# Optimization experiments

Hardware: AMD Instinct MI355X
Metric: run time of the kernel (lower is better)

Reference implementation:

```python
import jax, jax.numpy as jnp
import numpy as np

NUM_CLASSES = 19
RMI_RADIUS = 3
POOL_SIZE = 3
POOL_STRIDE = 3
IGNORE_INDEX = 255
LOSS_WEIGHT = 1.0


def _avg_pool_nchw(x, k, s):
    # torch F.avg_pool2d with padding=k//2, count_include_pad=True
    p = k // 2
    summed = jax.lax.reduce_window(
        x, 0.0, jax.lax.add,
        window_dimensions=(1, 1, k, k),
        window_strides=(1, 1, s, s),
        padding=[(0, 0), (0, 0), (p, p), (p, p)])
    return summed / float(k * k)


def _map_get_pairs(labels, probs, radius):
    h, w = labels.shape[2], labels.shape[3]
    nh, nw = h - radius + 1, w - radius + 1
    la = jnp.stack([labels[:, :, y:y + nh, x:x + nw]
                    for y in range(radius) for x in range(radius)], axis=2)
    pr = jnp.stack([probs[:, :, y:y + nh, x:x + nw]
                    for y in range(radius) for x in range(radius)], axis=2)
    return la, pr  # (N, C, r*r, nh, nw)


def _log_det_by_cholesky(mat):
    chol = jnp.linalg.cholesky(mat)
    diag = jnp.diagonal(chol, axis1=-2, axis2=-1)
    return 2.0 * jnp.sum(jnp.log(diag + 1e-8), axis=-1)


def _rmi_lower_bound(labels_4d, probs_4d):
    labels_4d = _avg_pool_nchw(labels_4d, POOL_SIZE, POOL_STRIDE)
    probs_4d = _avg_pool_nchw(probs_4d, POOL_SIZE, POOL_STRIDE)
    la, pr = _map_get_pairs(labels_4d, probs_4d, RMI_RADIUS)
    N, C, D = la.shape[:3]
    la = la.reshape(N, C, D, -1)   # (N, C, D, M)
    pr = pr.reshape(N, C, D, -1)
    M = la.shape[-1]
    la = la - la.mean(axis=-1, keepdims=True)
    pr = pr - pr.mean(axis=-1, keepdims=True)
    la_cov = jnp.einsum('ncdm,ncem->ncde', la, la) / M
    pr_cov = jnp.einsum('ncdm,ncem->ncde', pr, pr) / M
    pr_la_cov = jnp.einsum('ncdm,ncem->ncde', pr, la) / M
    eye = jnp.eye(D, dtype=la_cov.dtype)
    la_cov_inv = jnp.linalg.inv(la_cov + eye * 1e-5)
    appro_var = pr_cov - jnp.einsum('ncde,ncef,ncgf->ncdg',
                                    pr_la_cov, la_cov_inv, pr_la_cov)
    appro_var = appro_var + eye * 1e-6
    rmi_per_class = 0.5 * _log_det_by_cholesky(appro_var)  # (N, C)
    rmi_per_class = rmi_per_class.mean(axis=0)             # (C,)
    return jnp.sum(rmi_per_class) / NUM_CLASSES


def setup_inputs() -> dict:
    key = jax.random.key(0)
    k1, k2 = jax.random.split(key)
    cls_score = jax.random.normal(k1, (4, 19, 512, 512), dtype=jnp.float32)
    label = jax.random.randint(k2, (4, 512, 512), 0, NUM_CLASSES, dtype=jnp.int64)
    return {"cls_score": cls_score, "label": label}


def reference(cls_score, label):
    probs = jax.nn.softmax(cls_score.astype(jnp.float32), axis=1)
    valid = (label >= 0) & (label < NUM_CLASSES) & (label != IGNORE_INDEX)
    lbl = jnp.where(valid, label, 0)
    onehot = jax.nn.one_hot(lbl, NUM_CLASSES, dtype=jnp.float32)
    onehot = jnp.transpose(onehot, (0, 3, 1, 2))  # (N, C, H, W)
    vmask = valid[:, None, :, :].astype(jnp.float32)
    onehot = onehot * vmask
    probs = probs * vmask
    loss = _rmi_lower_bound(onehot, probs)
    return LOSS_WEIGHT * loss
```

## Files before the change

### kernel.cpp

```cpp
#include <hip/hip_runtime.h>
#include <math.h>

#define NBATCH 4
#define NCLS   19
#define HWDIM  512
#define HW     (512 * 512)
#define PH     171
#define PP2    (171 * 171)
#define NHW    169
#define MM     (169 * 169)
#define ZSPLIT 2

__global__ __launch_bounds__(512) void stage1_pool(
    const float* __restrict__ cls, const int* __restrict__ label,
    float* __restrict__ P, float* __restrict__ L) {
  int n  = blockIdx.x / PH;
  int ph = blockIdx.x - n * PH;
  int col = threadIdx.x;

  float accP[NCLS], accL[NCLS];
#pragma unroll
  for (int c = 0; c < NCLS; ++c) { accP[c] = 0.f; accL[c] = 0.f; }

#pragma unroll
  for (int i = 0; i < 3; ++i) {
    int r = 3 * ph - 1 + i;
    if (r < 0 || r >= HWDIM) continue;
    int lb = label[((size_t)n * HWDIM + r) * HWDIM + col];
    const float* base = cls + (size_t)n * NCLS * HW + (size_t)r * HWDIM + col;
    float v[NCLS];
    float mx = -INFINITY;
#pragma unroll
    for (int c = 0; c < NCLS; ++c) {
      v[c] = base[(size_t)c * HW];
      mx = fmaxf(mx, v[c]);
    }
    float se = 0.f;
#pragma unroll
    for (int c = 0; c < NCLS; ++c) {
      v[c] = expf(v[c] - mx);
      se += v[c];
    }
    if (lb >= 0 && lb < NCLS) {
      float inv = 1.f / se;
#pragma unroll
      for (int c = 0; c < NCLS; ++c) {
        accP[c] += v[c] * inv;
        accL[c] += (lb == c) ? 1.f : 0.f;
      }
    }
  }

  __shared__ float xbP[4][516];
  __shared__ float xbL[4][516];
  const float inv9 = 1.f / 9.f;
#pragma unroll
  for (int c0 = 0; c0 < NCLS; c0 += 4) {
    int nc_round = (NCLS - c0) < 4 ? (NCLS - c0) : 4;
#pragma unroll
    for (int cc = 0; cc < 4; ++cc) {
      if (cc < nc_round) {
        xbP[cc][1 + col] = accP[(c0 + cc) < NCLS ? (c0 + cc) : 0];
        xbL[cc][1 + col] = accL[(c0 + cc) < NCLS ? (c0 + cc) : 0];
        if (col == 0) { xbP[cc][0] = 0.f; xbL[cc][0] = 0.f; }
      }
    }
    __syncthreads();
    if (col < PH) {
      int pw = col;
#pragma unroll
      for (int cc = 0; cc < 4; ++cc) {
        if (cc < nc_round) {
          int c = c0 + cc;
          float sP = xbP[cc][3 * pw] + xbP[cc][3 * pw + 1] + xbP[cc][3 * pw + 2];
          float sL = xbL[cc][3 * pw] + xbL[cc][3 * pw + 1] + xbL[cc][3 * pw + 2];
          size_t o = ((size_t)(n * NCLS + c)) * PP2 + (size_t)ph * PH + pw;
          P[o] = sP * inv9;
          L[o] = sL * inv9;
        }
      }
    }
    __syncthreads();
  }
}

template <int PART>
__device__ __forceinline__ void mom_body(
    int nc, int z, const float* __restrict__ P, const float* __restrict__ L,
    float* __restrict__ covp, float* red) {
  constexpr int NA  = (PART == 0) ? 63 : (PART == 1 ? 45 : 81);
  constexpr int OFF = (PART == 0) ? 0  : (PART == 1 ? 63 : 108);
  const float* Pp = P + (size_t)nc * PP2;
  const float* Lp = L + (size_t)nc * PP2;

  float acc[NA];
#pragma unroll
  for (int k = 0; k < NA; ++k) acc[k] = 0.f;

  int task = threadIdx.x;
  if (task < 3 * NHW) {
    int ysub = task / NHW;
    int xx   = task - ysub * NHW;
    int base = z * 85;
    int rt   = (z == 0) ? 85 : (NHW - 85);
    int y0 = base + (rt * ysub) / 3;
    int y1 = base + (rt * (ysub + 1)) / 3;

    float wp[9], wl[9];
#pragma unroll
    for (int dy = 0; dy < 2; ++dy) {
#pragma unroll
      for (int dx = 0; dx < 3; ++dx) {
        wp[dy * 3 + dx] = Pp[(y0 + dy) * PH + xx + dx];
        if (PART != 1) wl[dy * 3 + dx] = Lp[(y0 + dy) * PH + xx + dx];
      }
    }
    for (int y = y0; y < y1; ++y) {
#pragma unroll
      for (int dx = 0; dx < 3; ++dx) {
        wp[6 + dx] = Pp[(y + 2) * PH + xx + dx];
        if (PART != 1) wl[6 + dx] = Lp[(y + 2) * PH + xx + dx];
      }
      if (PART == 0) {
#pragma unroll
        for (int d = 0; d < 9; ++d) {
          acc[d]     += wl[d];
          acc[9 + d] += wp[d];
        }
        int k = 18;
#pragma unroll
        for (int d = 0; d < 9; ++d)
#pragma unroll
          for (int e = d; e < 9; ++e) { acc[k] += wl[d] * wl[e]; ++k; }
      } else if (PART == 1) {
        int k = 0;
#pragma unroll
        for (int d = 0; d < 9; ++d)
#pragma unroll
          for (int e = d; e < 9; ++e) { acc[k] += wp[d] * wp[e]; ++k; }
      } else {
#pragma unroll
        for (int d = 0; d < 9; ++d)
#pragma unroll
          for (int e = 0; e < 9; ++e) acc[d * 9 + e] += wp[d] * wl[e];
      }
#pragma unroll
      for (int t = 0; t < 6; ++t) {
        wp[t] = wp[t + 3];
        if (PART != 1) wl[t] = wl[t + 3];
      }
    }
  }

  int lane = threadIdx.x & 63;
  int wid  = threadIdx.x >> 6;
#pragma unroll
  for (int k = 0; k < NA; ++k) {
    float v = acc[k];
#pragma unroll
    for (int o = 32; o > 0; o >>= 1) v += __shfl_down(v, o, 64);
    if (lane == 0) red[wid * NA + k] = v;
  }
  __syncthreads();
  if (threadIdx.x < NA) {
    float s = 0.f;
#pragma unroll
    for (int w = 0; w < 8; ++w) s += red[w * NA + threadIdx.x];
    covp[((size_t)z * NBATCH * NCLS + nc) * 192 + OFF + threadIdx.x] = s;
  }
}

__global__ __launch_bounds__(512) void stage2_mom(
    const float* __restrict__ P, const float* __restrict__ L,
    float* __restrict__ covp) {
  __shared__ float red[8 * 81];
  int nc = blockIdx.x;
  int z  = blockIdx.z;
  if (blockIdx.y == 0)      mom_body<0>(nc, z, P, L, covp, red);
  else if (blockIdx.y == 1) mom_body<1>(nc, z, P, L, covp, red);
  else                      mom_body<2>(nc, z, P, L, covp, red);
}

__global__ __launch_bounds__(64) void stage3_rmi(float* __restrict__ covp) {
  int nc  = blockIdx.x;
  int tid = threadIdx.x;
  const float* s0 = covp + (size_t)nc * 192;
  const float* s1 = covp + ((size_t)NBATCH * NCLS + nc) * 192;
  __shared__ double lc[81], pc[81], plc[81], mla[9], mpr[9];
  const double Minv = 1.0 / (double)MM;
#define LDM(k) ((double)s0[k] + (double)s1[k])

  if (tid < 9)       mla[tid]     = LDM(tid) * Minv;
  else if (tid < 18) mpr[tid - 9] = LDM(tid) * Minv;
  __syncthreads();

  for (int e = tid; e < 81; e += 64) {
    int r = e / 9, c = e - 9 * (e / 9);
    int lo = r < c ? r : c, hi = r < c ? c : r;
    int k = lo * 9 - lo * (lo - 1) / 2 + (hi - lo);
    double a = LDM(18 + k) * Minv - mla[r] * mla[c];
    if (r == c) a += 1e-5;
    lc[e] = a;
    pc[e] = LDM(63 + k) * Minv - mpr[r] * mpr[c];
    plc[e] = LDM(108 + e) * Minv - mpr[r] * mla[c];
  }
  __syncthreads();

  for (int j = 0; j < 9; ++j) {
    if (tid == 0) lc[j * 9 + j] = sqrt(lc[j * 9 + j]);
    __syncthreads();
    if (tid > j && tid < 9) lc[tid * 9 + j] /= lc[j * 9 + j];
    __syncthreads();
    if (tid > j && tid < 9) {
      double lij = lc[tid * 9 + j];
      for (int k = j + 1; k <= tid; ++k) lc[tid * 9 + k] -= lij * lc[k * 9 + j];
    }
    __syncthreads();
  }

  if (tid < 9) {
    int d = tid;
    for (int j = 0; j < 9; ++j) {
      double t = plc[d * 9 + j];
      for (int k = 0; k < j; ++k) t -= plc[d * 9 + k] * lc[j * 9 + k];
      plc[d * 9 + j] = t / lc[j * 9 + j];
    }
  }
  __syncthreads();

  for (int e = tid; e < 81; e += 64) {
    int r = e / 9, c = e - 9 * (e / 9);
    double a = pc[e];
    for (int f = 0; f < 9; ++f) a -= plc[r * 9 + f] * plc[c * 9 + f];
    if (r == c) a += 1e-6;
    pc[e] = a;
  }
  __syncthreads();

  for (int j = 0; j < 9; ++j) {
    if (tid == 0) pc[j * 9 + j] = sqrt(pc[j * 9 + j]);
    __syncthreads();
    if (tid > j && tid < 9) pc[tid * 9 + j] /= pc[j * 9 + j];
    __syncthreads();
    if (tid > j && tid < 9) {
      double lij = pc[tid * 9 + j];
      for (int k = j + 1; k <= tid; ++k) pc[tid * 9 + k] -= lij * pc[k * 9 + j];
    }
    __syncthreads();
  }

  if (tid == 0) {
    double sl = 0.0;
    for (int j = 0; j < 9; ++j) sl += log(pc[j * 9 + j] + 1e-8);
    *(double*)(covp + (size_t)nc * 192 + 190) = sl;
  }
#undef LDM
}

__global__ __launch_bounds__(64) void stage4_reduce(
    const float* __restrict__ covp, float* __restrict__ out) {
  int tid = threadIdx.x;
  double v = 0.0;
  if (tid < NBATCH * NCLS)
    v = *(const double*)(covp + (size_t)tid * 192 + 190);
  if (tid + 64 < NBATCH * NCLS)
    v += *(const double*)(covp + (size_t)(tid + 64) * 192 + 190);
#pragma unroll
  for (int o = 32; o > 0; o >>= 1) v += __shfl_down(v, o, 64);
  if (tid == 0) out[0] = (float)(v / (double)(NBATCH * NCLS));
}

extern "C" void kernel_launch(void* const* d_in, const int* in_sizes, int n_in,
                              void* d_out, int out_size, void* d_ws, size_t ws_size,
                              hipStream_t stream) {
  const float* cls  = (const float*)d_in[0];
  const int* label  = (const int*)d_in[1];
  float* out = (float*)d_out;

  float* P    = (float*)d_ws;
  float* L    = P + (size_t)NBATCH * NCLS * PP2;
  float* covp = L + (size_t)NBATCH * NCLS * PP2;

  stage1_pool<<<NBATCH * PH, 512, 0, stream>>>(cls, label, P, L);
  dim3 g2(NBATCH * NCLS, 3, ZSPLIT);
  stage2_mom<<<g2, 512, 0, stream>>>(P, L, covp);
  stage3_rmi<<<NBATCH * NCLS, 64, 0, stream>>>(covp);
  stage4_reduce<<<1, 64, 0, stream>>>(covp, out);
}
```

Before: 80.44 us.

## Vectorize stage1 softmax loads with float4 and prefetch next row in moment kernel

Stage1 now uses 384 threads, one per (row, 4-column) group, so each thread does float4 loads of the 19 class planes and the label row. The 3x3 pooling is done through shared memory covering all three input rows, one class per iteration. Stage2 prefetches the next window row into registers one iteration ahead to hide global load latency. In exchange, stage1 has more barriers (19 syncs) and each thread holds more registers (19 float4 values).

```diff
diff --git a/kernel.cpp b/kernel.cpp
--- a/kernel.cpp
+++ b/kernel.cpp
@@ -11,74 +11,91 @@
 #define MM     (169 * 169)
 #define ZSPLIT 2
 
-__global__ __launch_bounds__(512) void stage1_pool(
+typedef float f4 __attribute__((ext_vector_type(4)));
+
+__global__ __launch_bounds__(384) void stage1_pool(
     const float* __restrict__ cls, const int* __restrict__ label,
     float* __restrict__ P, float* __restrict__ L) {
-  int n  = blockIdx.x / PH;
-  int ph = blockIdx.x - n * PH;
-  int col = threadIdx.x;
-
-  float accP[NCLS], accL[NCLS];
-#pragma unroll
-  for (int c = 0; c < NCLS; ++c) { accP[c] = 0.f; accL[c] = 0.f; }
-
-#pragma unroll
-  for (int i = 0; i < 3; ++i) {
-    int r = 3 * ph - 1 + i;
-    if (r < 0 || r >= HWDIM) continue;
-    int lb = label[((size_t)n * HWDIM + r) * HWDIM + col];
-    const float* base = cls + (size_t)n * NCLS * HW + (size_t)r * HWDIM + col;
-    float v[NCLS];
-    float mx = -INFINITY;
+  int n   = blockIdx.x / PH;
+  int ph  = blockIdx.x - n * PH;
+  int t   = threadIdx.x;
+  int row = t >> 7;
+  int c4  = (t & 127) << 2;
+
+  int r = 3 * ph - 1 + row;
+  bool rowok = (r >= 0) && (r < HWDIM);
+
+  f4 v[NCLS];
+  f4 mx, se, inv;
+  int lb0 = -1, lb1 = -1, lb2 = -1, lb3 = -1;
+  f4 vmask = {0.f, 0.f, 0.f, 0.f};
+
+  if (rowok) {
+    const int4 lq = *(const int4*)(label + ((size_t)n * HWDIM + r) * HWDIM + c4);
+    lb0 = lq.x; lb1 = lq.y; lb2 = lq.z; lb3 = lq.w;
+    vmask.x = (lb0 >= 0 && lb0 < NCLS) ? 1.f : 0.f;
+    vmask.y = (lb1 >= 0 && lb1 < NCLS) ? 1.f : 0.f;
+    vmask.z = (lb2 >= 0 && lb2 < NCLS) ? 1.f : 0.f;
+    vmask.w = (lb3 >= 0 && lb3 < NCLS) ? 1.f : 0.f;
+
+    const float* base = cls + (size_t)n * NCLS * HW + (size_t)r * HWDIM + c4;
+#pragma unroll
+    for (int c = 0; c < NCLS; ++c)
+      v[c] = *(const f4*)(base + (size_t)c * HW);
+
+    mx = v[0];
+#pragma unroll
+    for (int c = 1; c < NCLS; ++c) {
+#pragma unroll
+      for (int j = 0; j < 4; ++j) mx[j] = fmaxf(mx[j], v[c][j]);
+    }
+    se = (f4){0.f, 0.f, 0.f, 0.f};
 #pragma unroll
     for (int c = 0; c < NCLS; ++c) {
-      v[c] = base[(size_t)c * HW];
-      mx = fmaxf(mx, v[c]);
-    }
-    float se = 0.f;
-#pragma unroll
-    for (int c = 0; c < NCLS; ++c) {
-      v[c] = expf(v[c] - mx);
-      se += v[c];
-    }
-    if (lb >= 0 && lb < NCLS) {
-      float inv = 1.f / se;
-#pragma unroll
-      for (int c = 0; c < NCLS; ++c) {
-        accP[c] += v[c] * inv;
-        accL[c] += (lb == c) ? 1.f : 0.f;
-      }
-    }
-  }
-
-  __shared__ float xbP[4][516];
-  __shared__ float xbL[4][516];
+#pragma unroll
+      for (int j = 0; j < 4; ++j) {
+        v[c][j] = expf(v[c][j] - mx[j]);
+        se[j] += v[c][j];
+      }
+    }
+#pragma unroll
+    for (int j = 0; j < 4; ++j) inv[j] = vmask[j] / se[j];
+  } else {
+#pragma unroll
+    for (int c = 0; c < NCLS; ++c) v[c] = (f4){0.f, 0.f, 0.f, 0.f};
+    inv = (f4){0.f, 0.f, 0.f, 0.f};
+  }
+
+  __shared__ float xbP[3][512];
+  __shared__ float xbL[3][512];
   const float inv9 = 1.f / 9.f;
-#pragma unroll
-  for (int c0 = 0; c0 < NCLS; c0 += 4) {
-    int nc_round = (NCLS - c0) < 4 ? (NCLS - c0) : 4;
-#pragma unroll
-    for (int cc = 0; cc < 4; ++cc) {
-      if (cc < nc_round) {
-        xbP[cc][1 + col] = accP[(c0 + cc) < NCLS ? (c0 + cc) : 0];
-        xbL[cc][1 + col] = accL[(c0 + cc) < NCLS ? (c0 + cc) : 0];
-        if (col == 0) { xbP[cc][0] = 0.f; xbL[cc][0] = 0.f; }
-      }
-    }
-    __syncthreads();
-    if (col < PH) {
-      int pw = col;
-#pragma unroll
-      for (int cc = 0; cc < 4; ++cc) {
-        if (cc < nc_round) {
-          int c = c0 + cc;
-          float sP = xbP[cc][3 * pw] + xbP[cc][3 * pw + 1] + xbP[cc][3 * pw + 2];
-          float sL = xbL[cc][3 * pw] + xbL[cc][3 * pw + 1] + xbL[cc][3 * pw + 2];
-          size_t o = ((size_t)(n * NCLS + c)) * PP2 + (size_t)ph * PH + pw;
-          P[o] = sP * inv9;
-          L[o] = sL * inv9;
-        }
-      }
+  int pw = t;
+
+#pragma unroll
+  for (int c = 0; c < NCLS; ++c) {
+    f4 pv, lv;
+#pragma unroll
+    for (int j = 0; j < 4; ++j) pv[j] = v[c][j] * inv[j];
+    lv.x = (lb0 == c) ? vmask.x : 0.f;
+    lv.y = (lb1 == c) ? vmask.y : 0.f;
+    lv.z = (lb2 == c) ? vmask.z : 0.f;
+    lv.w = (lb3 == c) ? vmask.w : 0.f;
+    *(f4*)&xbP[row][c4] = pv;
+    *(f4*)&xbL[row][c4] = lv;
+    __syncthreads();
+    if (pw < PH) {
+      int x0 = 3 * pw - 1;
+      float sP = 0.f, sL = 0.f;
+#pragma unroll
+      for (int i = 0; i < 3; ++i) {
+        float a = (pw > 0) ? xbP[i][x0] : 0.f;
+        float b = (pw > 0) ? xbL[i][x0] : 0.f;
+        sP += a + xbP[i][x0 + 1] + xbP[i][x0 + 2];
+        sL += b + xbL[i][x0 + 1] + xbL[i][x0 + 2];
+      }
+      size_t o = ((size_t)(n * NCLS + c)) * PP2 + (size_t)ph * PH + pw;
+      P[o] = sP * inv9;
+      L[o] = sL * inv9;
     }
     __syncthreads();
   }
@@ -106,7 +123,7 @@
     int y0 = base + (rt * ysub) / 3;
     int y1 = base + (rt * (ysub + 1)) / 3;
 
-    float wp[9], wl[9];
+    float wp[9], wl[9], pfp[3], pfl[3];
 #pragma unroll
     for (int dy = 0; dy < 2; ++dy) {
 #pragma unroll
@@ -115,11 +132,23 @@
         if (PART != 1) wl[dy * 3 + dx] = Lp[(y0 + dy) * PH + xx + dx];
       }
     }
+#pragma unroll
+    for (int dx = 0; dx < 3; ++dx) {
+      pfp[dx] = Pp[(y0 + 2) * PH + xx + dx];
+      if (PART != 1) pfl[dx] = Lp[(y0 + 2) * PH + xx + dx];
+    }
+
     for (int y = y0; y < y1; ++y) {
 #pragma unroll
       for (int dx = 0; dx < 3; ++dx) {
-        wp[6 + dx] = Pp[(y + 2) * PH + xx + dx];
-        if (PART != 1) wl[6 + dx] = Lp[(y + 2) * PH + xx + dx];
+        wp[6 + dx] = pfp[dx];
+        if (PART != 1) wl[6 + dx] = pfl[dx];
+      }
+      int yn = y + 3; if (yn > PH - 1) yn = PH - 1;
+#pragma unroll
+      for (int dx = 0; dx < 3; ++dx) {
+        pfp[dx] = Pp[yn * PH + xx + dx];
+        if (PART != 1) pfl[dx] = Lp[yn * PH + xx + dx];
       }
       if (PART == 0) {
 #pragma unroll
@@ -145,9 +174,9 @@
           for (int e = 0; e < 9; ++e) acc[d * 9 + e] += wp[d] * wl[e];
       }
 #pragma unroll
-      for (int t = 0; t < 6; ++t) {
-        wp[t] = wp[t + 3];
-        if (PART != 1) wl[t] = wl[t + 3];
+      for (int s = 0; s < 6; ++s) {
+        wp[s] = wp[s + 3];
+        if (PART != 1) wl[s] = wl[s + 3];
       }
     }
   }
@@ -281,7 +310,7 @@
   float* L    = P + (size_t)NBATCH * NCLS * PP2;
   float* covp = L + (size_t)NBATCH * NCLS * PP2;
 
-  stage1_pool<<<NBATCH * PH, 512, 0, stream>>>(cls, label, P, L);
+  stage1_pool<<<NBATCH * PH, 384, 0, stream>>>(cls, label, P, L);
   dim3 g2(NBATCH * NCLS, 3, ZSPLIT);
   stage2_mom<<<g2, 512, 0, stream>>>(P, L, covp);
   stage3_rmi<<<NBATCH * NCLS, 64, 0, stream>>>(covp);
```

Result: slower. 90.57 us (+12.6%).

## Split moment pass into six row bands staged through shared memory

Applied to the files above, without the earlier changes.

The moment-accumulation kernel now divides the 169 output rows into six bands instead of two, which triples the number of blocks. Each block first copies its band of pooled P and L rows (plus a two-row halo) into LDS, and the sliding-window loop then reads from shared memory instead of global memory. The RMI kernel now sums six partial records per (batch, class) instead of two. The aim is to fill more compute units and cut redundant global loads, at the price of about 42KB of LDS per block, a load-then-sync prologue, and more halo rows re-read across bands.

```diff
diff --git a/kernel.cpp b/kernel.cpp
--- a/kernel.cpp
+++ b/kernel.cpp
@@ -9,7 +9,8 @@
 #define PP2    (171 * 171)
 #define NHW    169
 #define MM     (169 * 169)
-#define ZSPLIT 2
+#define ZB     6
+#define HMAX   31
 
 __global__ __launch_bounds__(512) void stage1_pool(
     const float* __restrict__ cls, const int* __restrict__ label,
@@ -86,12 +87,10 @@
 
 template <int PART>
 __device__ __forceinline__ void mom_body(
-    int nc, int z, const float* __restrict__ P, const float* __restrict__ L,
-    float* __restrict__ covp, float* red) {
+    int bw, const float* sP, const float* sL,
+    float* __restrict__ covp, int rec, float* red) {
   constexpr int NA  = (PART == 0) ? 63 : (PART == 1 ? 45 : 81);
   constexpr int OFF = (PART == 0) ? 0  : (PART == 1 ? 63 : 108);
-  const float* Pp = P + (size_t)nc * PP2;
-  const float* Lp = L + (size_t)nc * PP2;
 
   float acc[NA];
 #pragma unroll
@@ -101,25 +100,23 @@
   if (task < 3 * NHW) {
     int ysub = task / NHW;
     int xx   = task - ysub * NHW;
-    int base = z * 85;
-    int rt   = (z == 0) ? 85 : (NHW - 85);
-    int y0 = base + (rt * ysub) / 3;
-    int y1 = base + (rt * (ysub + 1)) / 3;
+    int y0 = (bw * ysub) / 3;
+    int y1 = (bw * (ysub + 1)) / 3;
 
     float wp[9], wl[9];
 #pragma unroll
     for (int dy = 0; dy < 2; ++dy) {
 #pragma unroll
       for (int dx = 0; dx < 3; ++dx) {
-        wp[dy * 3 + dx] = Pp[(y0 + dy) * PH + xx + dx];
-        if (PART != 1) wl[dy * 3 + dx] = Lp[(y0 + dy) * PH + xx + dx];
+        wp[dy * 3 + dx] = sP[(y0 + dy) * PH + xx + dx];
+        if (PART != 1) wl[dy * 3 + dx] = sL[(y0 + dy) * PH + xx + dx];
       }
     }
     for (int y = y0; y < y1; ++y) {
 #pragma unroll
       for (int dx = 0; dx < 3; ++dx) {
-        wp[6 + dx] = Pp[(y + 2) * PH + xx + dx];
-        if (PART != 1) wl[6 + dx] = Lp[(y + 2) * PH + xx + dx];
+        wp[6 + dx] = sP[(y + 2) * PH + xx + dx];
+        if (PART != 1) wl[6 + dx] = sL[(y + 2) * PH + xx + dx];
       }
       if (PART == 0) {
 #pragma unroll
@@ -145,9 +142,9 @@
           for (int e = 0; e < 9; ++e) acc[d * 9 + e] += wp[d] * wl[e];
       }
 #pragma unroll
-      for (int t = 0; t < 6; ++t) {
-        wp[t] = wp[t + 3];
-        if (PART != 1) wl[t] = wl[t + 3];
+      for (int s = 0; s < 6; ++s) {
+        wp[s] = wp[s + 3];
+        if (PART != 1) wl[s] = wl[s + 3];
       }
     }
   }
@@ -166,29 +163,50 @@
     float s = 0.f;
 #pragma unroll
     for (int w = 0; w < 8; ++w) s += red[w * NA + threadIdx.x];
-    covp[((size_t)z * NBATCH * NCLS + nc) * 192 + OFF + threadIdx.x] = s;
+    covp[(size_t)rec * 192 + OFF + threadIdx.x] = s;
   }
 }
 
 __global__ __launch_bounds__(512) void stage2_mom(
     const float* __restrict__ P, const float* __restrict__ L,
     float* __restrict__ covp) {
+  __shared__ float sP[HMAX * PH];
+  __shared__ float sL[HMAX * PH];
   __shared__ float red[8 * 81];
   int nc = blockIdx.x;
+  int part = blockIdx.y;
   int z  = blockIdx.z;
-  if (blockIdx.y == 0)      mom_body<0>(nc, z, P, L, covp, red);
-  else if (blockIdx.y == 1) mom_body<1>(nc, z, P, L, covp, red);
-  else                      mom_body<2>(nc, z, P, L, covp, red);
+  int w0 = (NHW * z) / ZB;
+  int w1 = (NHW * (z + 1)) / ZB;
+  int bw = w1 - w0;
+  int tot = (bw + 2) * PH;
+
+  const float* Pp = P + (size_t)nc * PP2 + (size_t)w0 * PH;
+  const float* Lp = L + (size_t)nc * PP2 + (size_t)w0 * PH;
+  for (int i = threadIdx.x; i < tot; i += 512) {
+    sP[i] = Pp[i];
+    if (part != 1) sL[i] = Lp[i];
+  }
+  __syncthreads();
+
+  int rec = z * (NBATCH * NCLS) + nc;
+  if (part == 0)      mom_body<0>(bw, sP, sL, covp, rec, red);
+  else if (part == 1) mom_body<1>(bw, sP, sL, covp, rec, red);
+  else                mom_body<2>(bw, sP, sL, covp, rec, red);
 }
 
 __global__ __launch_bounds__(64) void stage3_rmi(float* __restrict__ covp) {
   int nc  = blockIdx.x;
   int tid = threadIdx.x;
-  const float* s0 = covp + (size_t)nc * 192;
-  const float* s1 = covp + ((size_t)NBATCH * NCLS + nc) * 192;
   __shared__ double lc[81], pc[81], plc[81], mla[9], mpr[9];
   const double Minv = 1.0 / (double)MM;
-#define LDM(k) ((double)s0[k] + (double)s1[k])
+
+#define LDM(k) ( (double)covp[(size_t)(0 * NBATCH * NCLS + nc) * 192 + (k)] \
+               + (double)covp[(size_t)(1 * NBATCH * NCLS + nc) * 192 + (k)] \
+               + (double)covp[(size_t)(2 * NBATCH * NCLS + nc) * 192 + (k)] \
+               + (double)covp[(size_t)(3 * NBATCH * NCLS + nc) * 192 + (k)] \
+               + (double)covp[(size_t)(4 * NBATCH * NCLS + nc) * 192 + (k)] \
+               + (double)covp[(size_t)(5 * NBATCH * NCLS + nc) * 192 + (k)] )
 
   if (tid < 9)       mla[tid]     = LDM(tid) * Minv;
   else if (tid < 18) mpr[tid - 9] = LDM(tid) * Minv;
@@ -282,7 +300,7 @@
   float* covp = L + (size_t)NBATCH * NCLS * PP2;
 
   stage1_pool<<<NBATCH * PH, 512, 0, stream>>>(cls, label, P, L);
-  dim3 g2(NBATCH * NCLS, 3, ZSPLIT);
+  dim3 g2(NBATCH * NCLS, 3, ZB);
   stage2_mom<<<g2, 512, 0, stream>>>(P, L, covp);
   stage3_rmi<<<NBATCH * NCLS, 64, 0, stream>>>(covp);
   stage4_reduce<<<1, 64, 0, stream>>>(covp, out);
```

Result: slower. 121.1 us (+50.6%).

## Tile moment kernel into 4-wide strips with vector loads and padded rows

Applied to the files above, without the earlier changes.

Stage1 now writes pooled maps with rows padded to 176 floats and zero-fills the pad columns. Stage2 gives each thread a 4-column by band-of-rows tile and reads the 3x6 window with float4/float2 loads, so each loaded row feeds four output columns. It also drops the two-way z split, so stage3 reads one partial instead of summing two. This cuts redundant global loads per output and the extra blocks, but leaves only 228 blocks and raises register pressure from the 18-element windows on top of up to 81 accumulators.

```diff
diff --git a/kernel.cpp b/kernel.cpp
--- a/kernel.cpp
+++ b/kernel.cpp
@@ -6,10 +6,15 @@
 #define HWDIM  512
 #define HW     (512 * 512)
 #define PH     171
-#define PP2    (171 * 171)
+#define PHP    176
+#define PP2A   (171 * 176)
 #define NHW    169
 #define MM     (169 * 169)
-#define ZSPLIT 2
+#define NBAND  11
+#define NSTRIP 43
+
+typedef float f4 __attribute__((ext_vector_type(4)));
+typedef float f2 __attribute__((ext_vector_type(2)));
 
 __global__ __launch_bounds__(512) void stage1_pool(
     const float* __restrict__ cls, const int* __restrict__ label,
@@ -74,11 +79,21 @@
           int c = c0 + cc;
           float sP = xbP[cc][3 * pw] + xbP[cc][3 * pw + 1] + xbP[cc][3 * pw + 2];
           float sL = xbL[cc][3 * pw] + xbL[cc][3 * pw + 1] + xbL[cc][3 * pw + 2];
-          size_t o = ((size_t)(n * NCLS + c)) * PP2 + (size_t)ph * PH + pw;
+          size_t o = ((size_t)(n * NCLS + c)) * PP2A + (size_t)ph * PHP + pw;
           P[o] = sP * inv9;
           L[o] = sL * inv9;
         }
       }
+    } else if (col < PHP) {
+#pragma unroll
+      for (int cc = 0; cc < 4; ++cc) {
+        if (cc < nc_round) {
+          int c = c0 + cc;
+          size_t o = ((size_t)(n * NCLS + c)) * PP2A + (size_t)ph * PHP + col;
+          P[o] = 0.f;
+          L[o] = 0.f;
+        }
+      }
     }
     __syncthreads();
   }
@@ -86,68 +101,98 @@
 
 template <int PART>
 __device__ __forceinline__ void mom_body(
-    int nc, int z, const float* __restrict__ P, const float* __restrict__ L,
-    float* __restrict__ covp, float* red) {
+    const float* __restrict__ Pp, const float* __restrict__ Lp,
+    float* __restrict__ covp, int nc, float* red) {
   constexpr int NA  = (PART == 0) ? 63 : (PART == 1 ? 45 : 81);
   constexpr int OFF = (PART == 0) ? 0  : (PART == 1 ? 63 : 108);
-  const float* Pp = P + (size_t)nc * PP2;
-  const float* Lp = L + (size_t)nc * PP2;
 
   float acc[NA];
 #pragma unroll
   for (int k = 0; k < NA; ++k) acc[k] = 0.f;
 
-  int task = threadIdx.x;
-  if (task < 3 * NHW) {
-    int ysub = task / NHW;
-    int xx   = task - ysub * NHW;
-    int base = z * 85;
-    int rt   = (z == 0) ? 85 : (NHW - 85);
-    int y0 = base + (rt * ysub) / 3;
-    int y1 = base + (rt * (ysub + 1)) / 3;
-
-    float wp[9], wl[9];
-#pragma unroll
-    for (int dy = 0; dy < 2; ++dy) {
-#pragma unroll
-      for (int dx = 0; dx < 3; ++dx) {
-        wp[dy * 3 + dx] = Pp[(y0 + dy) * PH + xx + dx];
-        if (PART != 1) wl[dy * 3 + dx] = Lp[(y0 + dy) * PH + xx + dx];
-      }
-    }
+  int tid = threadIdx.x;
+  if (tid < NSTRIP * NBAND) {
+    int b  = tid / NSTRIP;
+    int s  = tid - b * NSTRIP;
+    int x0 = 4 * s;
+    int y0 = (NHW * b) / NBAND;
+    int y1 = (NHW * (b + 1)) / NBAND;
+
+    float wp[18], wl[18];
+#pragma unroll
+    for (int r = 0; r < 3; ++r) {
+      const float* rp = Pp + (y0 + r) * PHP + x0;
+      *(f4*)&wp[r * 6]     = *(const f4*)rp;
+      *(f2*)&wp[r * 6 + 4] = *(const f2*)(rp + 4);
+      if (PART != 1) {
+        const float* rl = Lp + (y0 + r) * PHP + x0;
+        *(f4*)&wl[r * 6]     = *(const f4*)rl;
+        *(f2*)&wl[r * 6 + 4] = *(const f2*)(rl + 4);
+      }
+    }
+
     for (int y = y0; y < y1; ++y) {
-#pragma unroll
-      for (int dx = 0; dx < 3; ++dx) {
-        wp[6 + dx] = Pp[(y + 2) * PH + xx + dx];
-        if (PART != 1) wl[6 + dx] = Lp[(y + 2) * PH + xx + dx];
-      }
-      if (PART == 0) {
-#pragma unroll
-        for (int d = 0; d < 9; ++d) {
-          acc[d]     += wl[d];
-          acc[9 + d] += wp[d];
+      int yn = (y + 3 <= PH - 1) ? (y + 3) : (PH - 1);
+      const float* rp = Pp + yn * PHP + x0;
+      f4 tp4 = *(const f4*)rp;
+      f2 tp2 = *(const f2*)(rp + 4);
+      f4 tl4; f2 tl2;
+      if (PART != 1) {
+        const float* rl = Lp + yn * PHP + x0;
+        tl4 = *(const f4*)rl;
+        tl2 = *(const f2*)(rl + 4);
+      }
+#pragma unroll
+      for (int p = 0; p < 4; ++p) {
+        if (x0 + p < NHW) {
+          if (PART == 0) {
+#pragma unroll
+            for (int dy = 0; dy < 3; ++dy)
+#pragma unroll
+              for (int dx = 0; dx < 3; ++dx) {
+                int d = dy * 3 + dx;
+                acc[d]     += wl[dy * 6 + p + dx];
+                acc[9 + d] += wp[dy * 6 + p + dx];
+              }
+            int k = 18;
+#pragma unroll
+            for (int d = 0; d < 9; ++d)
+#pragma unroll
+              for (int e = d; e < 9; ++e) {
+                acc[k] += wl[(d / 3) * 6 + p + (d % 3)] *
+                          wl[(e / 3) * 6 + p + (e % 3)];
+                ++k;
+              }
+          } else if (PART == 1) {
+            int k = 0;
+#pragma unroll
+            for (int d = 0; d < 9; ++d)
+#pragma unroll
+              for (int e = d; e < 9; ++e) {
+                acc[k] += wp[(d / 3) * 6 + p + (d % 3)] *
+                          wp[(e / 3) * 6 + p + (e % 3)];
+                ++k;
+              }
+          } else {
+#pragma unroll
+            for (int d = 0; d < 9; ++d)
+#pragma unroll
+              for (int e = 0; e < 9; ++e)
+                acc[d * 9 + e] += wp[(d / 3) * 6 + p + (d % 3)] *
+                                  wl[(e / 3) * 6 + p + (e % 3)];
+          }
         }
-        int k = 18;
-#pragma unroll
-        for (int d = 0; d < 9; ++d)
-#pragma unroll
-          for (int e = d; e < 9; ++e) { acc[k] += wl[d] * wl[e]; ++k; }
-      } else if (PART == 1) {
-        int k = 0;
-#pragma unroll
-        for (int d = 0; d < 9; ++d)
-#pragma unroll
-          for (int e = d; e < 9; ++e) { acc[k] += wp[d] * wp[e]; ++k; }
-      } else {
-#pragma unroll
-        for (int d = 0; d < 9; ++d)
-#pragma unroll
-          for (int e = 0; e < 9; ++e) acc[d * 9 + e] += wp[d] * wl[e];
-      }
-#pragma unroll
-      for (int t = 0; t < 6; ++t) {
-        wp[t] = wp[t + 3];
-        if (PART != 1) wl[t] = wl[t + 3];
+      }
+#pragma unroll
+      for (int t = 0; t < 12; ++t) {
+        wp[t] = wp[t + 6];
+        if (PART != 1) wl[t] = wl[t + 6];
+      }
+      *(f4*)&wp[12] = tp4;
+      *(f2*)&wp[16] = tp2;
+      if (PART != 1) {
+        *(f4*)&wl[12] = tl4;
+        *(f2*)&wl[16] = tl2;
       }
     }
   }
@@ -163,10 +208,10 @@
   }
   __syncthreads();
   if (threadIdx.x < NA) {
-    float s = 0.f;
-#pragma unroll
-    for (int w = 0; w < 8; ++w) s += red[w * NA + threadIdx.x];
-    covp[((size_t)z * NBATCH * NCLS + nc) * 192 + OFF + threadIdx.x] = s;
+    float sm = 0.f;
+#pragma unroll
+    for (int w = 0; w < 8; ++w) sm += red[w * NA + threadIdx.x];
+    covp[(size_t)nc * 192 + OFF + threadIdx.x] = sm;
   }
 }
 
@@ -175,34 +220,33 @@
     float* __restrict__ covp) {
   __shared__ float red[8 * 81];
   int nc = blockIdx.x;
-  int z  = blockIdx.z;
-  if (blockIdx.y == 0)      mom_body<0>(nc, z, P, L, covp, red);
-  else if (blockIdx.y == 1) mom_body<1>(nc, z, P, L, covp, red);
-  else                      mom_body<2>(nc, z, P, L, covp, red);
+  const float* Pp = P + (size_t)nc * PP2A;
+  const float* Lp = L + (size_t)nc * PP2A;
+  if (blockIdx.y == 0)      mom_body<0>(Pp, Lp, covp, nc, red);
+  else if (blockIdx.y == 1) mom_body<1>(Pp, Lp, covp, nc, red);
+  else                      mom_body<2>(Pp, Lp, covp, nc, red);
 }
 
 __global__ __launch_bounds__(64) void stage3_rmi(float* __restrict__ covp) {
   int nc  = blockIdx.x;
   int tid = threadIdx.x;
-  const float* s0 = covp + (size_t)nc * 192;
-  const float* s1 = covp + ((size_t)NBATCH * NCLS + nc) * 192;
+  const float* s = covp + (size_t)nc * 192;
   __shared__ double lc[81], pc[81], plc[81], mla[9], mpr[9];
   const double Minv = 1.0 / (double)MM;
-#define LDM(k) ((double)s0[k] + (double)s1[k])
-
-  if (tid < 9)       mla[tid]     = LDM(tid) * Minv;
-  else if (tid < 18) mpr[tid - 9] = LDM(tid) * Minv;
+
+  if (tid < 9)       mla[tid]     = (double)s[tid] * Minv;
+  else if (tid < 18) mpr[tid - 9] = (double)s[tid] * Minv;
   __syncthreads();
 
   for (int e = tid; e < 81; e += 64) {
     int r = e / 9, c = e - 9 * (e / 9);
     int lo = r < c ? r : c, hi = r < c ? c : r;
     int k = lo * 9 - lo * (lo - 1) / 2 + (hi - lo);
-    double a = LDM(18 + k) * Minv - mla[r] * mla[c];
+    double a = (double)s[18 + k] * Minv - mla[r] * mla[c];
     if (r == c) a += 1e-5;
     lc[e] = a;
-    pc[e] = LDM(63 + k) * Minv - mpr[r] * mpr[c];
-    plc[e] = LDM(108 + e) * Minv - mpr[r] * mla[c];
+    pc[e] = (double)s[63 + k] * Minv - mpr[r] * mpr[c];
+    plc[e] = (double)s[108 + e] * Minv - mpr[r] * mla[c];
   }
   __syncthreads();
 
@@ -254,7 +298,6 @@
     for (int j = 0; j < 9; ++j) sl += log(pc[j * 9 + j] + 1e-8);
     *(double*)(covp + (size_t)nc * 192 + 190) = sl;
   }
-#undef LDM
 }
 
 __global__ __launch_bounds__(64) void stage4_reduce(
@@ -278,11 +321,11 @@
   float* out = (float*)d_out;
 
   float* P    = (float*)d_ws;
-  float* L    = P + (size_t)NBATCH * NCLS * PP2;
-  float* covp = L + (size_t)NBATCH * NCLS * PP2;
+  float* L    = P + (size_t)NBATCH * NCLS * PP2A;
+  float* covp = L + (size_t)NBATCH * NCLS * PP2A;
 
   stage1_pool<<<NBATCH * PH, 512, 0, stream>>>(cls, label, P, L);
-  dim3 g2(NBATCH * NCLS, 3, ZSPLIT);
+  dim3 g2(NBATCH * NCLS, 3, 1);
   stage2_mom<<<g2, 512, 0, stream>>>(P, L, covp);
   stage3_rmi<<<NBATCH * NCLS, 64, 0, stream>>>(covp);
   stage4_reduce<<<1, 64, 0, stream>>>(covp, out);
```

Measured after the change: 76.56 us. 1.05x faster.
